# Kernel optimization log

Hardware: AMD Instinct MI355X
Metric: run time of the kernel (lower is better)

## Reference

```python
import jax, jax.numpy as jnp
import numpy as np

B, L, D, H, DH = 2, 2048, 1024, 16, 64
EPS = 1e-5
ROPE_BASE = 10000.0


def _layernorm(x, w, b):
    mu = jnp.mean(x, axis=-1, keepdims=True)
    var = jnp.var(x, axis=-1, keepdims=True)
    y = (x - mu) * jax.lax.rsqrt(var + EPS)
    y = y * w
    if b is not None:
        y = y + b
    return y


def _rope(x):
    # x: [B, L, H, DH]; GPT-NeoX-style rotation over the full head dim
    inv_freq = 1.0 / (ROPE_BASE ** (jnp.arange(0, DH, 2, dtype=jnp.float32) / DH))  # [DH/2]
    t = jnp.arange(L, dtype=jnp.float32)
    freqs = jnp.outer(t, inv_freq)                       # [L, DH/2]
    cos = jnp.concatenate([jnp.cos(freqs)] * 2, axis=-1)[:, None, :]  # [L, 1, DH]
    sin = jnp.concatenate([jnp.sin(freqs)] * 2, axis=-1)[:, None, :]
    x1, x2 = jnp.split(x, 2, axis=-1)
    rot = jnp.concatenate([-x2, x1], axis=-1)
    return x * cos + rot * sin


def setup_inputs() -> dict:
    key = jax.random.key(0)
    ks = jax.random.split(key, 3)
    x = jax.random.normal(ks[0], (B, L, D), dtype=jnp.float32)
    w_qkv = jax.random.normal(ks[1], (3 * D, D), dtype=jnp.float32) * (D ** -0.5)
    w_out = jax.random.normal(ks[2], (D, D), dtype=jnp.float32) * (D ** -0.5)
    return {
        "x": x,
        "ln_w": jnp.ones((D,), jnp.float32),
        "ln_b": jnp.zeros((D,), jnp.float32),
        "w_qkv": w_qkv,
        "q_ln_w": jnp.ones((D,), jnp.float32),
        "k_ln_w": jnp.ones((D,), jnp.float32),
        "w_out": w_out,
    }


def reference(x, ln_w, ln_b, w_qkv, q_ln_w, k_ln_w, w_out):
    h = _layernorm(x, ln_w, ln_b)                         # [B, L, D]
    qkv = jnp.einsum("bld,ed->ble", h, w_qkv)            # [B, L, 3D]
    q, k, v = jnp.split(qkv, 3, axis=-1)
    q = _layernorm(q, q_ln_w, None)                       # weight-only per-token LN
    k = _layernorm(k, k_ln_w, None)
    q = _rope(q.reshape(B, L, H, DH))                     # [B, L, H, DH]
    k = _rope(k.reshape(B, L, H, DH))
    v = v.reshape(B, L, H, DH)
    ctx = jax.nn.dot_product_attention(q, k, v)           # [B, L, H, DH], scale 1/sqrt(DH)
    ctx = ctx.reshape(B, L, D)
    return jnp.einsum("bld,od->blo", ctx, w_out)
```

## Files before the change

kernel.cpp:

```cpp
#include <hip/hip_runtime.h>
#include <math.h>

#define BB 2
#define LL 2048
#define DD 1024
#define HH 16
#define DHD 64
#define NT (BB*LL)
#define D3 (3*DD)
#define D2 (2*DD)

typedef __bf16 bf16x8 __attribute__((ext_vector_type(8)));
typedef float  f32x4  __attribute__((ext_vector_type(4)));

__device__ __forceinline__ f32x4 mfma16(bf16x8 a, bf16x8 b, f32x4 c) {
    return __builtin_amdgcn_mfma_f32_16x16x32_bf16(a, b, c, 0, 0, 0);
}

__device__ __forceinline__ unsigned short f2bf(float f) {
    unsigned int u = __float_as_uint(f);
    u = (u + 0x7FFFu + ((u >> 16) & 1u)) >> 16;
    return (unsigned short)u;
}
__device__ __forceinline__ float bf2f(unsigned short s) {
    return __uint_as_float(((unsigned int)s) << 16);
}

__device__ __forceinline__ void gload16(const void* g, void* l) {
    __builtin_amdgcn_global_load_lds(
        (const __attribute__((address_space(1))) void*)g,
        (__attribute__((address_space(3))) void*)l, 16, 0, 0);
}

__device__ __forceinline__ float wred(float v) {
#pragma unroll
    for (int off = 32; off > 0; off >>= 1) v += __shfl_down(v, off, 64);
    return v;
}

__device__ __forceinline__ unsigned int pack_bf2(float p0, float p1) {
    const unsigned int u0 = __float_as_uint(p0) + 0x8000u;
    const unsigned int u1 = __float_as_uint(p1) + 0x8000u;
    return __builtin_amdgcn_perm(u1, u0, 0x07060302u);
}

__global__ __launch_bounds__(256) void ln_cvt_kernel(
        const float* __restrict__ x, const float* __restrict__ w,
        const float* __restrict__ b, unsigned short* __restrict__ h,
        const float* __restrict__ wq, unsigned short* __restrict__ wqb,
        const float* __restrict__ wo, unsigned short* __restrict__ wob) {
    const int bx = blockIdx.x;
    const int tid = threadIdx.x;
    if (bx >= NT) {
        int i = (bx - NT) * 256 + tid;
        const float* s; unsigned short* d;
        if (i < 786432) { s = wq; d = wqb; }
        else            { i -= 786432; s = wo; d = wob; }
        const float4 v = ((const float4*)s)[i];
        ((ushort4*)d)[i] = make_ushort4(f2bf(v.x), f2bf(v.y), f2bf(v.z), f2bf(v.w));
        return;
    }
    const float4 v = ((const float4*)(x + (size_t)bx * DD))[tid];
    float s = v.x + v.y + v.z + v.w;
    float ss = v.x*v.x + v.y*v.y + v.z*v.z + v.w*v.w;
    s = wred(s); ss = wred(ss);
    __shared__ float red[8];
    if ((tid & 63) == 0) { red[tid >> 6] = s; red[4 + (tid >> 6)] = ss; }
    __syncthreads();
    s  = red[0] + red[1] + red[2] + red[3];
    ss = red[4] + red[5] + red[6] + red[7];
    const float mu  = s * (1.0f / DD);
    const float inv = rsqrtf(ss * (1.0f / DD) - mu * mu + 1e-5f);
    const float4 wv = ((const float4*)w)[tid];
    const float4 bv = ((const float4*)b)[tid];
    *(ushort4*)(h + (size_t)bx * DD + tid * 4) = make_ushort4(
        f2bf((v.x - mu) * inv * wv.x + bv.x),
        f2bf((v.y - mu) * inv * wv.y + bv.y),
        f2bf((v.z - mu) * inv * wv.z + bv.z),
        f2bf((v.w - mu) * inv * wv.w + bv.w));
}

__global__ __launch_bounds__(256) void gemm_qkv(
        const unsigned short* __restrict__ A, const unsigned short* __restrict__ B,
        unsigned short* __restrict__ qk, unsigned short* __restrict__ vt) {
    const int K = DD;
    __shared__ unsigned short As[128 * 32];
    __shared__ unsigned short Bs[128 * 32];
    const int tid = threadIdx.x;
    const int w = tid >> 6, lane = tid & 63;
    const int l15 = lane & 15, quad = lane >> 4;
    const int wr = w >> 1, wc = w & 1;
    const int m0 = blockIdx.y << 7, n0 = blockIdx.x << 7;

    const int srow = w * 32 + (lane >> 2);
    const int skel = (lane & 3) << 3;
    const unsigned short* gA = A + (size_t)(m0 + srow) * K + skel;
    const unsigned short* gB = B + (size_t)(n0 + srow) * K + skel;
    unsigned short* lA = &As[w * 1024];
    unsigned short* lB = &Bs[w * 1024];

    f32x4 acc[4][4];
#pragma unroll
    for (int i = 0; i < 4; i++)
#pragma unroll
        for (int j = 0; j < 4; j++) acc[i][j] = (f32x4){0.f, 0.f, 0.f, 0.f};

    for (int k0 = 0; k0 < K; k0 += 32) {
        gload16(gA + k0,                 lA);
        gload16(gA + k0 + (size_t)16*K,  lA + 512);
        gload16(gB + k0,                 lB);
        gload16(gB + k0 + (size_t)16*K,  lB + 512);
        __syncthreads();
        bf16x8 af[4], bg[4];
#pragma unroll
        for (int i = 0; i < 4; i++) {
            af[i] = *(const bf16x8*)&As[(wr*64 + i*16 + l15) * 32 + quad*8];
            bg[i] = *(const bf16x8*)&Bs[(wc*64 + i*16 + l15) * 32 + quad*8];
        }
#pragma unroll
        for (int i = 0; i < 4; i++)
#pragma unroll
            for (int j = 0; j < 4; j++)
                acc[i][j] = mfma16(af[i], bg[j], acc[i][j]);
        __syncthreads();
    }
    if (n0 < D2) {
#pragma unroll
        for (int i = 0; i < 4; i++) {
            const int mrow = m0 + wr*64 + i*16 + quad*4;
#pragma unroll
            for (int j = 0; j < 4; j++) {
                const int ncol = n0 + wc*64 + j*16 + l15;
#pragma unroll
                for (int r = 0; r < 4; r++)
                    qk[(size_t)(mrow + r) * D2 + ncol] = f2bf(acc[i][j][r]);
            }
        }
    } else {
#pragma unroll
        for (int i = 0; i < 4; i++) {
            const int mrow = m0 + wr*64 + i*16 + quad*4;
            const int bb = mrow >> 11, l = mrow & (LL - 1);
#pragma unroll
            for (int j = 0; j < 4; j++) {
                const int nv = n0 + wc*64 + j*16 + l15 - D2;
                const int hh = nv >> 6, dh = nv & 63;
                *(ushort4*)&vt[((size_t)(bb*HH + hh) * DHD + dh) * LL + l] =
                    make_ushort4(f2bf(acc[i][j][0]), f2bf(acc[i][j][1]),
                                 f2bf(acc[i][j][2]), f2bf(acc[i][j][3]));
            }
        }
    }
}

__global__ __launch_bounds__(256) void gemm_out(
        const unsigned short* __restrict__ A, const unsigned short* __restrict__ B,
        float* __restrict__ C, int M, int N, int K) {
    __shared__ unsigned short As[64 * 32];
    __shared__ unsigned short Bs[128 * 32];
    const int tid = threadIdx.x;
    const int w = tid >> 6, lane = tid & 63;
    const int l15 = lane & 15, quad = lane >> 4;
    const int wr = w >> 1, wc = w & 1;
    const int m0 = blockIdx.y << 6, n0 = blockIdx.x << 7;
    const int skel = (lane & 3) << 3;
    const unsigned short* gA = A + (size_t)(m0 + w*16 + (lane >> 2)) * K + skel;
    const unsigned short* gB = B + (size_t)(n0 + w*32 + (lane >> 2)) * K + skel;
    unsigned short* lA = &As[w * 512];
    unsigned short* lB = &Bs[w * 1024];
    f32x4 acc[2][4];
#pragma unroll
    for (int i = 0; i < 2; i++)
#pragma unroll
        for (int j = 0; j < 4; j++) acc[i][j] = (f32x4){0.f, 0.f, 0.f, 0.f};
    for (int k0 = 0; k0 < K; k0 += 32) {
        gload16(gA + k0,                 lA);
        gload16(gB + k0,                 lB);
        gload16(gB + k0 + (size_t)16*K,  lB + 512);
        __syncthreads();
        bf16x8 af[2], bg[4];
#pragma unroll
        for (int i = 0; i < 2; i++)
            af[i] = *(const bf16x8*)&As[(wr*32 + i*16 + l15) * 32 + quad*8];
#pragma unroll
        for (int j = 0; j < 4; j++)
            bg[j] = *(const bf16x8*)&Bs[(wc*64 + j*16 + l15) * 32 + quad*8];
#pragma unroll
        for (int i = 0; i < 2; i++)
#pragma unroll
            for (int j = 0; j < 4; j++)
                acc[i][j] = mfma16(af[i], bg[j], acc[i][j]);
        __syncthreads();
    }
#pragma unroll
    for (int i = 0; i < 2; i++) {
        const int mrow = m0 + wr*32 + i*16 + quad*4;
#pragma unroll
        for (int j = 0; j < 4; j++) {
            const int ncol = n0 + wc*64 + j*16 + l15;
#pragma unroll
            for (int r = 0; r < 4; r++)
                C[(size_t)(mrow + r) * N + ncol] = acc[i][j][r];
        }
    }
}

__global__ __launch_bounds__(256) void qk_rope_kernel(
        const unsigned short* __restrict__ qk,
        const float* __restrict__ qw, const float* __restrict__ kw,
        unsigned short* __restrict__ qarr, unsigned short* __restrict__ karr) {
    const int t = blockIdx.x;
    const int l = t & (LL - 1), b = t >> 11;
    const int tid = threadIdx.x;
    const unsigned short* base = qk + (size_t)t * D2;
    const ushort4 qu = *(const ushort4*)(base + tid * 4);
    const ushort4 ku = *(const ushort4*)(base + DD + tid * 4);
    const float q[4] = {bf2f(qu.x), bf2f(qu.y), bf2f(qu.z), bf2f(qu.w)};
    const float k[4] = {bf2f(ku.x), bf2f(ku.y), bf2f(ku.z), bf2f(ku.w)};
    float sq = q[0]+q[1]+q[2]+q[3], ssq = q[0]*q[0]+q[1]*q[1]+q[2]*q[2]+q[3]*q[3];
    float sk = k[0]+k[1]+k[2]+k[3], ssk = k[0]*k[0]+k[1]*k[1]+k[2]*k[2]+k[3]*k[3];
    sq = wred(sq); ssq = wred(ssq); sk = wred(sk); ssk = wred(ssk);
    __shared__ float red[16];
    __shared__ float qs[DD], ks[DD];
    const int wid = tid >> 6;
    if ((tid & 63) == 0) { red[wid] = sq; red[4+wid] = ssq; red[8+wid] = sk; red[12+wid] = ssk; }
    __syncthreads();
    sq = red[0]+red[1]+red[2]+red[3];    ssq = red[4]+red[5]+red[6]+red[7];
    sk = red[8]+red[9]+red[10]+red[11];  ssk = red[12]+red[13]+red[14]+red[15];
    const float muq = sq * (1.f/DD), invq = rsqrtf(ssq*(1.f/DD) - muq*muq + 1e-5f);
    const float muk = sk * (1.f/DD), invk = rsqrtf(ssk*(1.f/DD) - muk*muk + 1e-5f);
    const float4 qwv = ((const float4*)qw)[tid];
    const float4 kwv = ((const float4*)kw)[tid];
    const float qwa[4] = {qwv.x, qwv.y, qwv.z, qwv.w};
    const float kwa[4] = {kwv.x, kwv.y, kwv.z, kwv.w};
    float qn[4], kn[4];
#pragma unroll
    for (int e = 0; e < 4; e++) {
        qn[e] = (q[e] - muq) * invq * qwa[e];
        kn[e] = (k[e] - muk) * invk * kwa[e];
    }
    *(float4*)&qs[tid*4] = make_float4(qn[0], qn[1], qn[2], qn[3]);
    *(float4*)&ks[tid*4] = make_float4(kn[0], kn[1], kn[2], kn[3]);
    __syncthreads();
    const int d = tid * 4, j0 = d & 63;
    const bool first = (j0 < 32);
    const int pt = first ? (tid + 8) : (tid - 8);
    const float4 qp4 = *(const float4*)&qs[pt*4];
    const float4 kp4 = *(const float4*)&ks[pt*4];
    const float qb[4] = {qp4.x, qp4.y, qp4.z, qp4.w};
    const float kb[4] = {kp4.x, kp4.y, kp4.z, kp4.w};
    const float lf = (float)l;
    const float QS = 0.125f * 1.44269504088896340736f;
    unsigned short oq[4], ok[4];
#pragma unroll
    for (int e = 0; e < 4; e++) {
        const float fi   = (float)((j0 & 31) + e);
        const float frev = __builtin_amdgcn_exp2f(fi * -0.41524101186092029f)
                         * 0.15915494309189535f;
        float rev = lf * frev;
        rev -= floorf(rev);
        const float sn = __builtin_amdgcn_sinf(rev);
        const float c  = __builtin_amdgcn_cosf(rev);
        float vq, vk;
        if (first) { vq = qn[e]*c - qb[e]*sn; vk = kn[e]*c - kb[e]*sn; }
        else       { vq = qn[e]*c + qb[e]*sn; vk = kn[e]*c + kb[e]*sn; }
        oq[e] = f2bf(vq * QS);
        ok[e] = f2bf(vk);
    }
    const int hh = tid >> 4;
    const int dh = (tid * 4) & 63;
    const size_t ro = ((size_t)(b*HH + hh) * LL + l) * DHD + dh;
    *(ushort4*)(qarr + ro) = make_ushort4(oq[0], oq[1], oq[2], oq[3]);
    *(ushort4*)(karr + ro) = make_ushort4(ok[0], ok[1], ok[2], ok[3]);
}

__global__ __launch_bounds__(256, 4) void attn_kernel(
        const unsigned short* __restrict__ qarr,
        const unsigned short* __restrict__ karr,
        const unsigned short* __restrict__ vt,
        unsigned short* __restrict__ ctxb) {
    const int x = blockIdx.x;
    const int bh = (x & 7) | ((x >> 8) << 3);
    const int qblk = (x >> 3) & 31;
    const int b = bh >> 4, hh = bh & 15;
    const int q0 = qblk << 6;
    const int tid = threadIdx.x, w = tid >> 6, lane = tid & 63;
    const int l15 = lane & 15, quad = lane >> 4;
    const int h  = w >> 1;
    const int wr = w & 1;

    __shared__ union {
        struct {
            unsigned short Ks[2 * 32 * 64];
            unsigned short Vs[2 * 64 * 32];
            unsigned short Pw[4][16][40];
        } m;
        struct {
            float red[64][64];
            float lred[64];
            unsigned short red_bf[64][72];
        } e;
    } sm;

    const unsigned short* kbase = karr + ((size_t)bh * LL + h * 1024) * DHD;
    const unsigned short* vbase = vt   + (size_t)bh * DHD * LL + h * 1024;

    bf16x8 qf[2][2];
    {
        const unsigned short* qp = qarr + ((size_t)bh*LL + q0 + wr*32 + l15) * DHD + quad*8;
#pragma unroll
        for (int qt = 0; qt < 2; qt++)
#pragma unroll
            for (int c = 0; c < 2; c++)
                qf[qt][c] = *(const bf16x8*)(qp + qt*16*DHD + c*32);
    }

    bf16x8 ones;
#pragma unroll
    for (int i = 0; i < 8; i++) ones[i] = (__bf16)1.0f;

    const int p = w & 1;
    f32x4 o[2][4], lacc[2];
#pragma unroll
    for (int qt = 0; qt < 2; qt++) {
        lacc[qt] = (f32x4){0.f, 0.f, 0.f, 0.f};
#pragma unroll
        for (int nt = 0; nt < 4; nt++) o[qt][nt] = (f32x4){0.f, 0.f, 0.f, 0.f};
    }

    const int kr8 = lane >> 3, kc = lane & 7;
    const int vr4 = lane >> 2, vc = lane & 3;
#define STAGE(KT)                                                                   \
    {                                                                               \
        const int kt_ = (KT);                                                       \
        _Pragma("unroll")                                                           \
        for (int rd = 0; rd < 2; rd++) {                                            \
            const int row = p*16 + rd*8 + kr8;                                      \
            gload16(kbase + (size_t)(kt_*32 + row) * DHD + (kc ^ kr8) * 8,          \
                    &sm.m.Ks[h*2048 + (p*16 + rd*8) * 64]);                         \
        }                                                                           \
        _Pragma("unroll")                                                           \
        for (int rv = 0; rv < 2; rv++) {                                            \
            const int dhrow = p*32 + rv*16 + vr4;                                   \
            gload16(vbase + (size_t)dhrow * LL + kt_*32 + (vc ^ (vr4 & 3)) * 8,     \
                    &sm.m.Vs[h*2048 + (p*32 + rv*16) * 32]);                        \
        }                                                                           \
    }

    STAGE(0);

    for (int kt = 0; kt < 32; kt++) {
        __syncthreads();
        bf16x8 kf[2][2], vf[4];
#pragma unroll
        for (int t = 0; t < 2; t++)
#pragma unroll
            for (int c = 0; c < 2; c++) {
                const int slot = (quad + c*4) ^ (l15 & 7);
                kf[t][c] = *(const bf16x8*)&sm.m.Ks[h*2048 + (t*16 + l15) * 64 + slot*8];
            }
#pragma unroll
        for (int nt = 0; nt < 4; nt++) {
            const int slot = quad ^ (l15 & 3);
            vf[nt] = *(const bf16x8*)&sm.m.Vs[h*2048 + (nt*16 + l15) * 32 + slot*8];
        }
        __syncthreads();
        if (kt + 1 < 32) STAGE(kt + 1);

#pragma unroll
        for (int qt = 0; qt < 2; qt++) {
            f32x4 st[2];
#pragma unroll
            for (int t = 0; t < 2; t++) {
                f32x4 z = (f32x4){-64.f, -64.f, -64.f, -64.f};
                z = mfma16(kf[t][0], qf[qt][0], z);
                z = mfma16(kf[t][1], qf[qt][1], z);
                st[t] = z;
            }
#pragma unroll
            for (int t = 0; t < 2; t++) {
                const float p0 = __builtin_amdgcn_exp2f(st[t][0]);
                const float p1 = __builtin_amdgcn_exp2f(st[t][1]);
                const float p2 = __builtin_amdgcn_exp2f(st[t][2]);
                const float p3 = __builtin_amdgcn_exp2f(st[t][3]);
                uint2 pk;
                pk.x = pack_bf2(p0, p1);
                pk.y = pack_bf2(p2, p3);
                *(uint2*)&sm.m.Pw[w][l15][t*16 + quad*4] = pk;
            }
            const bf16x8 ap = *(const bf16x8*)&sm.m.Pw[w][l15][quad*8];
            lacc[qt] = mfma16(ap, ones, lacc[qt]);
#pragma unroll
            for (int nt = 0; nt < 4; nt++)
                o[qt][nt] = mfma16(ap, vf[nt], o[qt][nt]);
        }
    }
#undef STAGE

    __syncthreads();
    if (h == 1) {
#pragma unroll
        for (int qt = 0; qt < 2; qt++) {
#pragma unroll
            for (int nt = 0; nt < 4; nt++)
#pragma unroll
                for (int r = 0; r < 4; r++)
                    sm.e.red[wr*32 + qt*16 + quad*4 + r][nt*16 + l15] = o[qt][nt][r];
            if (l15 == 0)
#pragma unroll
                for (int r = 0; r < 4; r++)
                    sm.e.lred[wr*32 + qt*16 + quad*4 + r] = lacc[qt][r];
        }
    }
    __syncthreads();
    if (h == 0) {
#pragma unroll
        for (int qt = 0; qt < 2; qt++) {
            float inv[4];
#pragma unroll
            for (int r = 0; r < 4; r++)
                inv[r] = 1.0f / (lacc[qt][r] + sm.e.lred[wr*32 + qt*16 + quad*4 + r]);
#pragma unroll
            for (int nt = 0; nt < 4; nt++)
#pragma unroll
                for (int r = 0; r < 4; r++) {
                    const int tok = wr*32 + qt*16 + quad*4 + r;
                    const float v = (o[qt][nt][r] + sm.e.red[tok][nt*16 + l15]) * inv[r];
                    sm.e.red_bf[tok][nt*16 + l15] = f2bf(v);
                }
        }
    }
    __syncthreads();
#pragma unroll
    for (int i = 0; i < 2; i++) {
        const int idx = tid + 256*i;
        const int token = idx >> 3, ch = idx & 7;
        const uint4 vdat = *(const uint4*)&sm.e.red_bf[token][ch*8];
        *(uint4*)&ctxb[(size_t)(b*LL + q0 + token) * DD + hh*DHD + ch*8] = vdat;
    }
}

extern "C" void kernel_launch(void* const* d_in, const int* in_sizes, int n_in,
                              void* d_out, int out_size, void* d_ws, size_t ws_size,
                              hipStream_t stream) {
    const float* x      = (const float*)d_in[0];
    const float* ln_w   = (const float*)d_in[1];
    const float* ln_b   = (const float*)d_in[2];
    const float* w_qkv  = (const float*)d_in[3];
    const float* q_ln_w = (const float*)d_in[4];
    const float* k_ln_w = (const float*)d_in[5];
    const float* w_out  = (const float*)d_in[6];
    float* out = (float*)d_out;

    char* ws = (char*)d_ws;
    unsigned short* hb    = (unsigned short*)ws;
    unsigned short* karr  = (unsigned short*)ws;
    unsigned short* qk    = (unsigned short*)(ws + ((size_t)8  << 20));
    unsigned short* ctxb  = (unsigned short*)(ws + ((size_t)8  << 20));
    unsigned short* vtp   = (unsigned short*)(ws + ((size_t)24 << 20));
    unsigned short* qarr  = (unsigned short*)(ws + ((size_t)32 << 20));
    unsigned short* wqb   = (unsigned short*)(ws + ((size_t)40 << 20));
    unsigned short* wob   = (unsigned short*)(ws + ((size_t)46 << 20));

    ln_cvt_kernel<<<NT + 4096, 256, 0, stream>>>(x, ln_w, ln_b, hb,
                                                 w_qkv, wqb, w_out, wob);
    gemm_qkv<<<dim3(D3/128, NT/128), 256, 0, stream>>>(hb, wqb, qk, vtp);
    qk_rope_kernel<<<NT, 256, 0, stream>>>(qk, q_ln_w, k_ln_w, qarr, karr);
    attn_kernel<<<1024, 256, 0, stream>>>(qarr, karr, vtp, ctxb);
    gemm_out<<<dim3(DD/128, NT/64), 256, 0, stream>>>(ctxb, wob, out, NT, DD, DD);
}
```

Baseline: 249.1 us.

## Enlarge attention tiles to 128 queries and 64-key steps, sum row totals in registers

```diff
diff --git a/kernel.cpp b/kernel.cpp
--- a/kernel.cpp
+++ b/kernel.cpp
@@ -274,157 +274,160 @@
     *(ushort4*)(karr + ro) = make_ushort4(ok[0], ok[1], ok[2], ok[3]);
 }
 
-__global__ __launch_bounds__(256, 4) void attn_kernel(
+__global__ __launch_bounds__(256, 2) void attn_kernel(
         const unsigned short* __restrict__ qarr,
         const unsigned short* __restrict__ karr,
         const unsigned short* __restrict__ vt,
         unsigned short* __restrict__ ctxb) {
     const int x = blockIdx.x;
-    const int bh = (x & 7) | ((x >> 8) << 3);
-    const int qblk = (x >> 3) & 31;
+    const int bh = (x & 7) | ((x >> 7) << 3);
+    const int qblk = (x >> 3) & 15;
     const int b = bh >> 4, hh = bh & 15;
-    const int q0 = qblk << 6;
+    const int q0 = qblk << 7;
     const int tid = threadIdx.x, w = tid >> 6, lane = tid & 63;
     const int l15 = lane & 15, quad = lane >> 4;
-    const int h  = w >> 1;
-    const int wr = w & 1;
+    const int h  = w & 1;
+    const int wq = w >> 1;
 
     __shared__ union {
         struct {
-            unsigned short Ks[2 * 32 * 64];
-            unsigned short Vs[2 * 64 * 32];
-            unsigned short Pw[4][16][40];
+            unsigned short Ks[2][64 * 64];
+            unsigned short Vs[2][64 * 64];
+            unsigned short Pw[4][16][72];
         } m;
         struct {
-            float red[64][64];
-            float lred[64];
-            unsigned short red_bf[64][72];
+            float red[128][68];
+            float lred[2][128];
+            unsigned short red_bf[128][72];
         } e;
     } sm;
 
     const unsigned short* kbase = karr + ((size_t)bh * LL + h * 1024) * DHD;
     const unsigned short* vbase = vt   + (size_t)bh * DHD * LL + h * 1024;
 
-    bf16x8 qf[2][2];
+    bf16x8 qf[4][2];
     {
-        const unsigned short* qp = qarr + ((size_t)bh*LL + q0 + wr*32 + l15) * DHD + quad*8;
-#pragma unroll
-        for (int qt = 0; qt < 2; qt++)
+        const unsigned short* qp = qarr + ((size_t)bh*LL + q0 + wq*64 + l15) * DHD + quad*8;
+#pragma unroll
+        for (int qt = 0; qt < 4; qt++)
 #pragma unroll
             for (int c = 0; c < 2; c++)
                 qf[qt][c] = *(const bf16x8*)(qp + qt*16*DHD + c*32);
     }
 
-    bf16x8 ones;
-#pragma unroll
-    for (int i = 0; i < 8; i++) ones[i] = (__bf16)1.0f;
-
-    const int p = w & 1;
-    f32x4 o[2][4], lacc[2];
-#pragma unroll
-    for (int qt = 0; qt < 2; qt++) {
-        lacc[qt] = (f32x4){0.f, 0.f, 0.f, 0.f};
+    f32x4 o[4][4];
+    float lacc[4] = {0.f, 0.f, 0.f, 0.f};
+#pragma unroll
+    for (int qt = 0; qt < 4; qt++)
 #pragma unroll
         for (int nt = 0; nt < 4; nt++) o[qt][nt] = (f32x4){0.f, 0.f, 0.f, 0.f};
-    }
-
-    const int kr8 = lane >> 3, kc = lane & 7;
-    const int vr4 = lane >> 2, vc = lane & 3;
-#define STAGE(KT)                                                                   \
-    {                                                                               \
-        const int kt_ = (KT);                                                       \
-        _Pragma("unroll")                                                           \
-        for (int rd = 0; rd < 2; rd++) {                                            \
-            const int row = p*16 + rd*8 + kr8;                                      \
-            gload16(kbase + (size_t)(kt_*32 + row) * DHD + (kc ^ kr8) * 8,          \
-                    &sm.m.Ks[h*2048 + (p*16 + rd*8) * 64]);                         \
-        }                                                                           \
-        _Pragma("unroll")                                                           \
-        for (int rv = 0; rv < 2; rv++) {                                            \
-            const int dhrow = p*32 + rv*16 + vr4;                                   \
-            gload16(vbase + (size_t)dhrow * LL + kt_*32 + (vc ^ (vr4 & 3)) * 8,     \
-                    &sm.m.Vs[h*2048 + (p*32 + rv*16) * 32]);                        \
-        }                                                                           \
+
+    const int r8 = lane >> 3, c8 = lane & 7;
+#define STAGE(KT)                                                                  \
+    {                                                                              \
+        const int kt_ = (KT);                                                      \
+        _Pragma("unroll")                                                          \
+        for (int rd = 0; rd < 4; rd++) {                                           \
+            const int row = wq*32 + rd*8 + r8;                                     \
+            gload16(kbase + (size_t)(kt_*64 + row) * DHD + ((c8 ^ r8) << 3),       \
+                    &sm.m.Ks[h][(wq*32 + rd*8) * 64]);                             \
+            gload16(vbase + (size_t)row * LL + kt_*64 + ((c8 ^ r8) << 3),          \
+                    &sm.m.Vs[h][(wq*32 + rd*8) * 64]);                             \
+        }                                                                          \
     }
 
     STAGE(0);
 
-    for (int kt = 0; kt < 32; kt++) {
-        __syncthreads();
-        bf16x8 kf[2][2], vf[4];
-#pragma unroll
-        for (int t = 0; t < 2; t++)
+    for (int kt = 0; kt < 16; kt++) {
+        __syncthreads();
+        bf16x8 kf[4][2], vf[4][2];
+#pragma unroll
+        for (int t = 0; t < 4; t++)
 #pragma unroll
             for (int c = 0; c < 2; c++) {
                 const int slot = (quad + c*4) ^ (l15 & 7);
-                kf[t][c] = *(const bf16x8*)&sm.m.Ks[h*2048 + (t*16 + l15) * 64 + slot*8];
-            }
-#pragma unroll
-        for (int nt = 0; nt < 4; nt++) {
-            const int slot = quad ^ (l15 & 3);
-            vf[nt] = *(const bf16x8*)&sm.m.Vs[h*2048 + (nt*16 + l15) * 32 + slot*8];
-        }
-        __syncthreads();
-        if (kt + 1 < 32) STAGE(kt + 1);
-
-#pragma unroll
-        for (int qt = 0; qt < 2; qt++) {
-            f32x4 st[2];
-#pragma unroll
-            for (int t = 0; t < 2; t++) {
+                kf[t][c] = *(const bf16x8*)&sm.m.Ks[h][(t*16 + l15) * 64 + slot*8];
+                vf[t][c] = *(const bf16x8*)&sm.m.Vs[h][(t*16 + l15) * 64 + slot*8];
+            }
+        __syncthreads();
+        if (kt + 1 < 16) STAGE(kt + 1);
+
+#pragma unroll
+        for (int qt = 0; qt < 4; qt++) {
+            f32x4 st[4];
+#pragma unroll
+            for (int t = 0; t < 4; t++) {
                 f32x4 z = (f32x4){-64.f, -64.f, -64.f, -64.f};
                 z = mfma16(kf[t][0], qf[qt][0], z);
                 z = mfma16(kf[t][1], qf[qt][1], z);
                 st[t] = z;
             }
-#pragma unroll
-            for (int t = 0; t < 2; t++) {
+            float ps = 0.f;
+#pragma unroll
+            for (int t = 0; t < 4; t++) {
                 const float p0 = __builtin_amdgcn_exp2f(st[t][0]);
                 const float p1 = __builtin_amdgcn_exp2f(st[t][1]);
                 const float p2 = __builtin_amdgcn_exp2f(st[t][2]);
                 const float p3 = __builtin_amdgcn_exp2f(st[t][3]);
+                ps += (p0 + p1) + (p2 + p3);
                 uint2 pk;
                 pk.x = pack_bf2(p0, p1);
                 pk.y = pack_bf2(p2, p3);
                 *(uint2*)&sm.m.Pw[w][l15][t*16 + quad*4] = pk;
             }
-            const bf16x8 ap = *(const bf16x8*)&sm.m.Pw[w][l15][quad*8];
-            lacc[qt] = mfma16(ap, ones, lacc[qt]);
+            lacc[qt] += ps;
+            const bf16x8 ap0 = *(const bf16x8*)&sm.m.Pw[w][l15][quad*8];
+            const bf16x8 ap1 = *(const bf16x8*)&sm.m.Pw[w][l15][32 + quad*8];
+#pragma unroll
+            for (int nt = 0; nt < 4; nt++) {
+                f32x4 t0 = o[qt][nt];
+                t0 = mfma16(ap0, vf[nt][0], t0);
+                t0 = mfma16(ap1, vf[nt][1], t0);
+                o[qt][nt] = t0;
+            }
+        }
+    }
+#undef STAGE
+
+    float lq[4];
+#pragma unroll
+    for (int qt = 0; qt < 4; qt++) {
+        float v = lacc[qt];
+        v += __shfl_xor(v, 16);
+        v += __shfl_xor(v, 32);
+        lq[qt] = v;
+    }
+
+    __syncthreads();
+    if (h == 1) {
+#pragma unroll
+        for (int qt = 0; qt < 4; qt++) {
 #pragma unroll
             for (int nt = 0; nt < 4; nt++)
-                o[qt][nt] = mfma16(ap, vf[nt], o[qt][nt]);
-        }
-    }
-#undef STAGE
-
-    __syncthreads();
-    if (h == 1) {
-#pragma unroll
-        for (int qt = 0; qt < 2; qt++) {
+#pragma unroll
+                for (int r = 0; r < 4; r++)
+                    sm.e.red[wq*64 + qt*16 + quad*4 + r][nt*16 + l15] = o[qt][nt][r];
+        }
+    }
+    if (quad == 0)
+#pragma unroll
+        for (int qt = 0; qt < 4; qt++)
+            sm.e.lred[h][wq*64 + qt*16 + l15] = lq[qt];
+    __syncthreads();
+    if (h == 0) {
+#pragma unroll
+        for (int qt = 0; qt < 4; qt++) {
+            float inv[4];
+#pragma unroll
+            for (int r = 0; r < 4; r++) {
+                const int tok = wq*64 + qt*16 + quad*4 + r;
+                inv[r] = 1.0f / (sm.e.lred[0][tok] + sm.e.lred[1][tok]);
+            }
 #pragma unroll
             for (int nt = 0; nt < 4; nt++)
 #pragma unroll
-                for (int r = 0; r < 4; r++)
-                    sm.e.red[wr*32 + qt*16 + quad*4 + r][nt*16 + l15] = o[qt][nt][r];
-            if (l15 == 0)
-#pragma unroll
-                for (int r = 0; r < 4; r++)
-                    sm.e.lred[wr*32 + qt*16 + quad*4 + r] = lacc[qt][r];
-        }
-    }
-    __syncthreads();
-    if (h == 0) {
-#pragma unroll
-        for (int qt = 0; qt < 2; qt++) {
-            float inv[4];
-#pragma unroll
-            for (int r = 0; r < 4; r++)
-                inv[r] = 1.0f / (lacc[qt][r] + sm.e.lred[wr*32 + qt*16 + quad*4 + r]);
-#pragma unroll
-            for (int nt = 0; nt < 4; nt++)
-#pragma unroll
                 for (int r = 0; r < 4; r++) {
-                    const int tok = wr*32 + qt*16 + quad*4 + r;
+                    const int tok = wq*64 + qt*16 + quad*4 + r;
                     const float v = (o[qt][nt][r] + sm.e.red[tok][nt*16 + l15]) * inv[r];
                     sm.e.red_bf[tok][nt*16 + l15] = f2bf(v);
                 }
@@ -432,7 +435,7 @@
     }
     __syncthreads();
 #pragma unroll
-    for (int i = 0; i < 2; i++) {
+    for (int i = 0; i < 4; i++) {
         const int idx = tid + 256*i;
         const int token = idx >> 3, ch = idx & 7;
         const uint4 vdat = *(const uint4*)&sm.e.red_bf[token][ch*8];
@@ -466,6 +469,6 @@
                                                  w_qkv, wqb, w_out, wob);
     gemm_qkv<<<dim3(D3/128, NT/128), 256, 0, stream>>>(hb, wqb, qk, vtp);
     qk_rope_kernel<<<NT, 256, 0, stream>>>(qk, q_ln_w, k_ln_w, qarr, karr);
-    attn_kernel<<<1024, 256, 0, stream>>>(qarr, karr, vtp, ctxb);
+    attn_kernel<<<512, 256, 0, stream>>>(qarr, karr, vtp, ctxb);
     gemm_out<<<dim3(DD/128, NT/64), 256, 0, stream>>>(ctxb, wob, out, NT, DD, DD);
 }
```

Measured after the change: 228.4 us. 1.09x faster.

## Double-buffer K/V tiles and shuffle P via bpermute in attention

Applied to the files above, without the earlier changes.

```diff
diff --git a/kernel.cpp b/kernel.cpp
--- a/kernel.cpp
+++ b/kernel.cpp
@@ -286,18 +286,17 @@
     const int q0 = qblk << 6;
     const int tid = threadIdx.x, w = tid >> 6, lane = tid & 63;
     const int l15 = lane & 15, quad = lane >> 4;
-    const int h  = w >> 1;
-    const int wr = w & 1;
+    const int h  = w & 1;
+    const int wq = w >> 1;
 
     __shared__ union {
         struct {
-            unsigned short Ks[2 * 32 * 64];
-            unsigned short Vs[2 * 64 * 32];
-            unsigned short Pw[4][16][40];
+            unsigned short Ks[2][2][32 * 64];
+            unsigned short Vs[2][2][64 * 32];
         } m;
         struct {
-            float red[64][64];
-            float lred[64];
+            float red[64][68];
+            float lred[2][64];
             unsigned short red_bf[64][72];
         } e;
     } sm;
@@ -307,7 +306,7 @@
 
     bf16x8 qf[2][2];
     {
-        const unsigned short* qp = qarr + ((size_t)bh*LL + q0 + wr*32 + l15) * DHD + quad*8;
+        const unsigned short* qp = qarr + ((size_t)bh*LL + q0 + wq*32 + l15) * DHD + quad*8;
 #pragma unroll
         for (int qt = 0; qt < 2; qt++)
 #pragma unroll
@@ -315,57 +314,56 @@
                 qf[qt][c] = *(const bf16x8*)(qp + qt*16*DHD + c*32);
     }
 
-    bf16x8 ones;
-#pragma unroll
-    for (int i = 0; i < 8; i++) ones[i] = (__bf16)1.0f;
-
-    const int p = w & 1;
-    f32x4 o[2][4], lacc[2];
-#pragma unroll
-    for (int qt = 0; qt < 2; qt++) {
-        lacc[qt] = (f32x4){0.f, 0.f, 0.f, 0.f};
+    f32x4 o[2][4];
+    float lacc[2] = {0.f, 0.f};
+#pragma unroll
+    for (int qt = 0; qt < 2; qt++)
 #pragma unroll
         for (int nt = 0; nt < 4; nt++) o[qt][nt] = (f32x4){0.f, 0.f, 0.f, 0.f};
-    }
-
-    const int kr8 = lane >> 3, kc = lane & 7;
-    const int vr4 = lane >> 2, vc = lane & 3;
-#define STAGE(KT)                                                                   \
+
+    const int kr8 = lane >> 3, kc8 = lane & 7;
+    const int vr4 = lane >> 2, vc4 = lane & 3;
+    const int idxA = (l15 + 32*(quad & 1)) * 4;
+    const int idxB = idxA + 64;
+
+#define STAGE(KT, BUF)                                                              \
     {                                                                               \
         const int kt_ = (KT);                                                       \
         _Pragma("unroll")                                                           \
         for (int rd = 0; rd < 2; rd++) {                                            \
-            const int row = p*16 + rd*8 + kr8;                                      \
-            gload16(kbase + (size_t)(kt_*32 + row) * DHD + (kc ^ kr8) * 8,          \
-                    &sm.m.Ks[h*2048 + (p*16 + rd*8) * 64]);                         \
+            const int row = wq*16 + rd*8 + kr8;                                     \
+            gload16(kbase + (size_t)(kt_*32 + row) * DHD + ((kc8 ^ (row & 7)) << 3),\
+                    &sm.m.Ks[h][BUF][(wq*16 + rd*8) * 64]);                         \
         }                                                                           \
         _Pragma("unroll")                                                           \
         for (int rv = 0; rv < 2; rv++) {                                            \
-            const int dhrow = p*32 + rv*16 + vr4;                                   \
-            gload16(vbase + (size_t)dhrow * LL + kt_*32 + (vc ^ (vr4 & 3)) * 8,     \
-                    &sm.m.Vs[h*2048 + (p*32 + rv*16) * 32]);                        \
+            const int row = wq*32 + rv*16 + vr4;                                    \
+            gload16(vbase + (size_t)row * LL + kt_*32 + ((vc4 ^ ((row >> 1) & 3)) << 3),\
+                    &sm.m.Vs[h][BUF][(wq*32 + rv*16) * 32]);                        \
         }                                                                           \
     }
 
-    STAGE(0);
+    STAGE(0, 0);
 
     for (int kt = 0; kt < 32; kt++) {
         __syncthreads();
+        if (kt + 1 < 32) STAGE(kt + 1, (kt + 1) & 1);
+        const int bb = kt & 1;
+
         bf16x8 kf[2][2], vf[4];
 #pragma unroll
         for (int t = 0; t < 2; t++)
 #pragma unroll
             for (int c = 0; c < 2; c++) {
                 const int slot = (quad + c*4) ^ (l15 & 7);
-                kf[t][c] = *(const bf16x8*)&sm.m.Ks[h*2048 + (t*16 + l15) * 64 + slot*8];
-            }
-#pragma unroll
-        for (int nt = 0; nt < 4; nt++) {
-            const int slot = quad ^ (l15 & 3);
-            vf[nt] = *(const bf16x8*)&sm.m.Vs[h*2048 + (nt*16 + l15) * 32 + slot*8];
-        }
-        __syncthreads();
-        if (kt + 1 < 32) STAGE(kt + 1);
+                kf[t][c] = *(const bf16x8*)&sm.m.Ks[h][bb][(t*16 + l15) * 64 + slot*8];
+            }
+        {
+            const int slotv = quad ^ ((l15 >> 1) & 3);
+#pragma unroll
+            for (int nt = 0; nt < 4; nt++)
+                vf[nt] = *(const bf16x8*)&sm.m.Vs[h][bb][(nt*16 + l15) * 32 + slotv*8];
+        }
 
 #pragma unroll
         for (int qt = 0; qt < 2; qt++) {
@@ -377,54 +375,77 @@
                 z = mfma16(kf[t][1], qf[qt][1], z);
                 st[t] = z;
             }
+            uint2 pk[2];
+            float ps = 0.f;
 #pragma unroll
             for (int t = 0; t < 2; t++) {
                 const float p0 = __builtin_amdgcn_exp2f(st[t][0]);
                 const float p1 = __builtin_amdgcn_exp2f(st[t][1]);
                 const float p2 = __builtin_amdgcn_exp2f(st[t][2]);
                 const float p3 = __builtin_amdgcn_exp2f(st[t][3]);
-                uint2 pk;
-                pk.x = pack_bf2(p0, p1);
-                pk.y = pack_bf2(p2, p3);
-                *(uint2*)&sm.m.Pw[w][l15][t*16 + quad*4] = pk;
-            }
-            const bf16x8 ap = *(const bf16x8*)&sm.m.Pw[w][l15][quad*8];
-            lacc[qt] = mfma16(ap, ones, lacc[qt]);
+                ps += (p0 + p1) + (p2 + p3);
+                pk[t].x = pack_bf2(p0, p1);
+                pk[t].y = pack_bf2(p2, p3);
+            }
+            lacc[qt] += ps;
+            const int a0x = __builtin_amdgcn_ds_bpermute(idxA, (int)pk[0].x);
+            const int a1x = __builtin_amdgcn_ds_bpermute(idxA, (int)pk[1].x);
+            const int a0y = __builtin_amdgcn_ds_bpermute(idxA, (int)pk[0].y);
+            const int a1y = __builtin_amdgcn_ds_bpermute(idxA, (int)pk[1].y);
+            const int b0x = __builtin_amdgcn_ds_bpermute(idxB, (int)pk[0].x);
+            const int b1x = __builtin_amdgcn_ds_bpermute(idxB, (int)pk[1].x);
+            const int b0y = __builtin_amdgcn_ds_bpermute(idxB, (int)pk[0].y);
+            const int b1y = __builtin_amdgcn_ds_bpermute(idxB, (int)pk[1].y);
+            union { int u[4]; bf16x8 v; } ap;
+            ap.u[0] = (quad < 2) ? a0x : a1x;
+            ap.u[1] = (quad < 2) ? a0y : a1y;
+            ap.u[2] = (quad < 2) ? b0x : b1x;
+            ap.u[3] = (quad < 2) ? b0y : b1y;
 #pragma unroll
             for (int nt = 0; nt < 4; nt++)
-                o[qt][nt] = mfma16(ap, vf[nt], o[qt][nt]);
+                o[qt][nt] = mfma16(ap.v, vf[nt], o[qt][nt]);
         }
     }
 #undef STAGE
 
+    float lq[2];
+#pragma unroll
+    for (int qt = 0; qt < 2; qt++) {
+        float v = lacc[qt];
+        v += __shfl_xor(v, 16);
+        v += __shfl_xor(v, 32);
+        lq[qt] = v;
+    }
+
     __syncthreads();
     if (h == 1) {
 #pragma unroll
-        for (int qt = 0; qt < 2; qt++) {
+        for (int qt = 0; qt < 2; qt++)
 #pragma unroll
             for (int nt = 0; nt < 4; nt++)
 #pragma unroll
                 for (int r = 0; r < 4; r++)
-                    sm.e.red[wr*32 + qt*16 + quad*4 + r][nt*16 + l15] = o[qt][nt][r];
-            if (l15 == 0)
-#pragma unroll
-                for (int r = 0; r < 4; r++)
-                    sm.e.lred[wr*32 + qt*16 + quad*4 + r] = lacc[qt][r];
-        }
-    }
+                    sm.e.red[wq*32 + qt*16 + quad*4 + r][nt*16 + l15] = o[qt][nt][r];
+    }
+    if (quad == 0)
+#pragma unroll
+        for (int qt = 0; qt < 2; qt++)
+            sm.e.lred[h][wq*32 + qt*16 + l15] = lq[qt];
     __syncthreads();
     if (h == 0) {
 #pragma unroll
         for (int qt = 0; qt < 2; qt++) {
             float inv[4];
 #pragma unroll
-            for (int r = 0; r < 4; r++)
-                inv[r] = 1.0f / (lacc[qt][r] + sm.e.lred[wr*32 + qt*16 + quad*4 + r]);
+            for (int r = 0; r < 4; r++) {
+                const int tok = wq*32 + qt*16 + quad*4 + r;
+                inv[r] = 1.0f / (sm.e.lred[0][tok] + sm.e.lred[1][tok]);
+            }
 #pragma unroll
             for (int nt = 0; nt < 4; nt++)
 #pragma unroll
                 for (int r = 0; r < 4; r++) {
-                    const int tok = wr*32 + qt*16 + quad*4 + r;
+                    const int tok = wq*32 + qt*16 + quad*4 + r;
                     const float v = (o[qt][nt][r] + sm.e.red[tok][nt*16 + l15]) * inv[r];
                     sm.e.red_bf[tok][nt*16 + l15] = f2bf(v);
                 }
```

Result: no change. 251.6 us (+1.0%).
